# Kernel tuning notes

Measured on AMD Instinct MI355X. Metric: run time of the kernel, lower is better.

## Reference

```python
import jax, jax.numpy as jnp
import numpy as np

FP8_MAX = 448.0  # max normal for float8_e4m3fn
BLOCK = 128


def setup_inputs() -> dict:
    key = jax.random.key(0)
    k1, k2, k3 = jax.random.split(key, 3)
    B, S, D_IN, D_OUT = 2, 2048, 4096, 8192
    x = jax.random.normal(k1, (B, S, D_IN), dtype=jnp.float32)
    # stored weight is fp8_e4m3fn; materialize as f32 values that are exactly fp8-representable
    w = jax.random.normal(k2, (D_OUT, D_IN), dtype=jnp.float32)
    weight = w.astype(jnp.float8_e4m3fn).astype(jnp.float32)
    # positive per-(128x128)-block dequant scales
    weight_scale_inv = (
        jax.random.uniform(k3, (D_OUT // BLOCK, D_IN // BLOCK), dtype=jnp.float32) * 0.05 + 0.005
    )
    return {"x": x, "weight": weight, "weight_scale_inv": weight_scale_inv}


def _quantize_per_token(x2d):
    # x2d: [M, K] -> fp8 values + [M, 1] f32 scale
    amax = jnp.clip(jnp.max(jnp.abs(x2d), axis=-1, keepdims=True), min=1e-12)
    x_scale = (amax / FP8_MAX).astype(jnp.float32)
    x_fp8 = (x2d / x_scale).astype(jnp.float8_e4m3fn)
    return x_fp8, x_scale


def _dequantize_weight(weight, weight_scale_inv):
    # weight: [O, K] (fp8-representable f32), scales: [O/B, K/B]
    O, K = weight.shape
    w_fp8 = weight.astype(jnp.float8_e4m3fn).astype(jnp.float32)
    wb = w_fp8.reshape(O // BLOCK, BLOCK, K // BLOCK, BLOCK)
    wb = wb * weight_scale_inv[:, None, :, None]
    return wb.reshape(O, K)


def reference(x, weight, weight_scale_inv):
    orig_shape = x.shape
    x2d = x.reshape(-1, orig_shape[-1])  # [M, K], M > 1 path
    x_fp8, x_scale = _quantize_per_token(x2d)
    # block-scaled fp8 GEMM: y[m,n] = x_scale[m] * sum_k x_fp8[m,k] * w_fp8[n,k] * s[n//B,k//B]
    w_deq = _dequantize_weight(weight, weight_scale_inv)  # [O, K]
    y = jnp.einsum("mk,ok->mo", x_fp8.astype(jnp.float32), w_deq) * x_scale
    return y.reshape(*orig_shape[:-1], weight.shape[0])
```

## Files before the change

### kernel.cpp

```cpp
#include <hip/hip_runtime.h>

typedef float f32x4  __attribute__((ext_vector_type(4)));
typedef float f32x16 __attribute__((ext_vector_type(16)));
typedef int   i32x4  __attribute__((ext_vector_type(4)));
typedef int   i32x8  __attribute__((ext_vector_type(8)));

#define AS1 __attribute__((address_space(1)))
#define AS3 __attribute__((address_space(3)))

__global__ __launch_bounds__(256) void quant_x_fp8_kernel(
    const float* __restrict__ x, unsigned char* __restrict__ x8,
    float* __restrict__ xs, int K) {
  int m = blockIdx.x;
  int t = threadIdx.x;
  const f32x4* src = (const f32x4*)(x + (size_t)m * K + t * 16);
  f32x4 v[4];
  float am = 0.0f;
#pragma unroll
  for (int i = 0; i < 4; ++i) {
    v[i] = src[i];
#pragma unroll
    for (int j = 0; j < 4; ++j) am = fmaxf(am, __builtin_fabsf(v[i][j]));
  }
#pragma unroll
  for (int off = 32; off >= 1; off >>= 1)
    am = fmaxf(am, __shfl_xor(am, off, 64));
  __shared__ float red[4];
  int wv = t >> 6, lane = t & 63;
  if (lane == 0) red[wv] = am;
  __syncthreads();
  am = fmaxf(fmaxf(red[0], red[1]), fmaxf(red[2], red[3]));
  am = fmaxf(am, 1e-12f);
  float sc = am / 448.0f;
  if (t == 0) xs[m] = sc;
  i32x4 out;
#pragma unroll
  for (int i = 0; i < 4; ++i) {
    float q0 = v[i][0] / sc, q1 = v[i][1] / sc;
    float q2 = v[i][2] / sc, q3 = v[i][3] / sc;
    int p = __builtin_amdgcn_cvt_pk_fp8_f32(q0, q1, 0, false);
    p = __builtin_amdgcn_cvt_pk_fp8_f32(q2, q3, p, true);
    out[i] = p;
  }
  *(i32x4*)(x8 + (size_t)m * K + t * 16) = out;
}

__global__ __launch_bounds__(256) void quant_w_fp8_kernel(
    const float* __restrict__ w, unsigned char* __restrict__ w8) {
  size_t idx = (size_t)blockIdx.x * 256 + threadIdx.x;
  const f32x4* src = (const f32x4*)w + idx * 4;
  i32x4 out;
#pragma unroll
  for (int i = 0; i < 4; ++i) {
    f32x4 v = src[i];
    int p = __builtin_amdgcn_cvt_pk_fp8_f32(v[0], v[1], 0, false);
    p = __builtin_amdgcn_cvt_pk_fp8_f32(v[2], v[3], p, true);
    out[i] = p;
  }
  ((i32x4*)w8)[idx] = out;
}

__global__ __launch_bounds__(256, 2) void gemm_mxfp8_kernel(
    const unsigned char* __restrict__ A8,
    const unsigned char* __restrict__ W8,
    const float* __restrict__ xs,
    const float* __restrict__ wsinv,
    float* __restrict__ Y,
    int M, int N, int K) {
  const int KB = K >> 7;

  int bid = blockIdx.x, nwg = gridDim.x;
  int wg = (bid & 7) * (nwg >> 3) + (bid >> 3);
  int mt = M >> 8;
  int bm = wg & (mt - 1);
  int bn = wg / mt;
  int m0 = bm << 8, n0 = bn << 7;

  __shared__ __align__(16) char lds[49152];

  const int tid = threadIdx.x, wv = tid >> 6, lane = tid & 63;
  const int wr = wv >> 1, wc = wv & 1;
  const int l31 = lane & 31, hi2 = lane >> 5;

  const int lineB = (l31 >> 1) * 128;
  const int par4 = (l31 & 1) << 2;
  const int xr = (l31 >> 1) & 7;
  const int s0 = 2 * hi2, s1 = 2 * hi2 + 1;
  const int aL = wr * 8192 + lineB + ((par4 | s0) ^ xr) * 16;
  const int aH = wr * 8192 + lineB + ((par4 | s1) ^ xr) * 16;
  const int bL = wc * 4096 + lineB + ((par4 | s0) ^ xr) * 16;
  const int bH = wc * 4096 + lineB + ((par4 | s1) ^ xr) * 16;

  const int stgD = tid << 4;
  const int inv = (tid & 7) ^ ((tid >> 3) & 7);
  const int rLoc = 2 * (tid >> 3) + (inv >> 2);
  const int cSrc = (inv & 3) << 4;
  const size_t rowB = (size_t)K;
  const size_t g64r = 64 * rowB;
  const char* pA = (const char*)A8 + (size_t)(m0 + rLoc) * rowB + cSrc;
  const char* pB = (const char*)W8 + (size_t)(n0 + rLoc) * rowB + cSrc;

  const float* wsv = wsinv + (size_t)bn * KB;

  f32x16 acc[4][2];
#pragma unroll
  for (int i = 0; i < 4; ++i)
#pragma unroll
    for (int j = 0; j < 2; ++j) acc[i][j] = (f32x16)0.0f;

  i32x8 af, bf[2];

#define GL(SRC, DST)                                                           \
  __builtin_amdgcn_global_load_lds((const AS1 void*)(SRC), (AS3 void*)(DST),   \
                                   16, 0, 0)
#define STG_A(COND, SB, SRC)                                                   \
  if (COND) {                                                                  \
    const char* s_ = (SRC);                                                    \
    char* d_ = lds + (SB) + stgD;                                              \
    GL(s_, d_);                                                                \
    GL(s_ + g64r, d_ + 4096);                                                  \
    GL(s_ + 2 * g64r, d_ + 8192);                                              \
    GL(s_ + 3 * g64r, d_ + 12288);                                             \
  }
#define STG_B(COND, SB, SRC)                                                   \
  if (COND) {                                                                  \
    const char* s_ = (SRC);                                                    \
    char* d_ = lds + (SB) + 16384 + stgD;                                      \
    GL(s_, d_);                                                                \
    GL(s_ + g64r, d_ + 4096);                                                  \
  }

#define RD_A(RB, MJ)                                                           \
  {                                                                            \
    const char* p_ = lds + (RB) + (MJ) * 2048;                                 \
    i32x4 lo = *(const i32x4*)(p_ + aL);                                       \
    i32x4 hi = *(const i32x4*)(p_ + aH);                                       \
    af = __builtin_shufflevector(lo, hi, 0, 1, 2, 3, 4, 5, 6, 7);              \
  }
#define RD_B(RB, NJ)                                                           \
  {                                                                            \
    const char* p_ = lds + (RB) + 16384 + (NJ) * 2048;                         \
    i32x4 lo = *(const i32x4*)(p_ + bL);                                       \
    i32x4 hi = *(const i32x4*)(p_ + bH);                                       \
    bf[NJ] = __builtin_shufflevector(lo, hi, 0, 1, 2, 3, 4, 5, 6, 7);          \
  }

#define MMFF(MJ, NJ, R_)                                                       \
  {                                                                            \
    _Pragma("unroll") for (int q = 0; q < 16; ++q)                             \
        acc[MJ][NJ][q] *= (R_);                                                \
    acc[MJ][NJ] = __builtin_amdgcn_mfma_scale_f32_32x32x64_f8f6f4(             \
        af, bf[NJ], acc[MJ][NJ], 0, 0, 0, 0x7f7f7f7f, 0, 0x7f7f7f7f);          \
  }
#define MMFD(MJ, NJ)                                                           \
  acc[MJ][NJ] = __builtin_amdgcn_mfma_scale_f32_32x32x64_f8f6f4(               \
      af, bf[NJ], acc[MJ][NJ], 0, 0, 0, 0x7f7f7f7f, 0, 0x7f7f7f7f);

#define BODY_CORE(MM0, MM1, MM2, MM3, RD, ST, G)                               \
  {                                                                            \
    RD_B(RD, 0);                                                               \
    RD_B(RD, 1);                                                               \
    RD_A(RD, 0);                                                               \
    STG_A(G, ST, pAs);                                                         \
    __builtin_amdgcn_s_setprio(1);                                             \
    MM0;                                                                       \
    __builtin_amdgcn_s_setprio(0);                                             \
    STG_B(G, ST, pBs);                                                         \
    RD_A(RD, 1);                                                               \
    __builtin_amdgcn_s_setprio(1);                                             \
    MM1;                                                                       \
    __builtin_amdgcn_s_setprio(0);                                             \
    RD_A(RD, 2);                                                               \
    __builtin_amdgcn_s_setprio(1);                                             \
    MM2;                                                                       \
    __builtin_amdgcn_s_setprio(0);                                             \
    RD_A(RD, 3);                                                               \
    __builtin_amdgcn_s_setprio(1);                                             \
    MM3;                                                                       \
    __builtin_amdgcn_s_setprio(0);                                             \
    asm volatile("s_waitcnt vmcnt(0)" ::: "memory");                           \
    __builtin_amdgcn_s_barrier();                                              \
    pAs += 64;                                                                 \
    pBs += 64;                                                                 \
  }

#define BODY_E(T, G)                                                           \
  {                                                                            \
    float sc_ = wsv[(T)];                                                      \
    float r_ = sp_ / sc_;                                                      \
    sp_ = sc_;                                                                 \
    BODY_CORE(MMFF(0, 0, r_); MMFF(0, 1, r_), MMFF(1, 0, r_); MMFF(1, 1, r_),  \
              MMFF(2, 0, r_); MMFF(2, 1, r_), MMFF(3, 0, r_); MMFF(3, 1, r_),  \
              0, 24576, G)                                                     \
  }
#define BODY_O(G)                                                              \
  BODY_CORE(MMFD(0, 0); MMFD(0, 1), MMFD(1, 0); MMFD(1, 1),                    \
            MMFD(2, 0); MMFD(2, 1), MMFD(3, 0); MMFD(3, 1), 24576, 0, G)

  STG_A(true, 0, pA);
  STG_B(true, 0, pB);
  asm volatile("s_waitcnt vmcnt(0)" ::: "memory");
  __builtin_amdgcn_s_barrier();

  const char* pAs = pA + 64;
  const char* pBs = pB + 64;
  float sp_ = wsv[0];

#pragma unroll 1
  for (int t = 0; t < KB; ++t) {
    BODY_E(t, true)
    BODY_O(t < KB - 1)
  }

#undef BODY_O
#undef BODY_E
#undef BODY_CORE
#undef MMFD
#undef MMFF
#undef RD_B
#undef RD_A
#undef STG_B
#undef STG_A
#undef GL

  const float sl_ = sp_;
#pragma unroll
  for (int mj = 0; mj < 4; ++mj)
#pragma unroll
    for (int nj = 0; nj < 2; ++nj) {
      int col = n0 + wc * 64 + nj * 32 + l31;
#pragma unroll
      for (int q = 0; q < 4; ++q) {
        int row0 = m0 + wr * 128 + mj * 32 + q * 8 + hi2 * 4;
        f32x4 sv = *(const f32x4*)(xs + row0);
#pragma unroll
        for (int j = 0; j < 4; ++j)
          Y[(size_t)(row0 + j) * N + col] = acc[mj][nj][q * 4 + j] * sv[j] * sl_;
      }
    }
}

extern "C" void kernel_launch(void* const* d_in, const int* in_sizes, int n_in,
                              void* d_out, int out_size, void* d_ws, size_t ws_size,
                              hipStream_t stream) {
  const float* x     = (const float*)d_in[0];
  const float* w     = (const float*)d_in[1];
  const float* wsinv = (const float*)d_in[2];
  float* y = (float*)d_out;

  const int K = 4096;
  const int M = in_sizes[0] / K;
  const int N = in_sizes[1] / K;

  unsigned char* x8 = (unsigned char*)d_ws;
  float* xs = (float*)((char*)d_ws + (size_t)M * K);
  unsigned char* w8 =
      (unsigned char*)d_ws + (size_t)M * K + (size_t)M * 4;

  quant_x_fp8_kernel<<<M, 256, 0, stream>>>(x, x8, xs, K);
  quant_w_fp8_kernel<<<(int)(((size_t)N * K / 16 + 255) / 256), 256, 0,
                       stream>>>(w, w8);

  dim3 grid((M / 256) * (N / 128));
  gemm_mxfp8_kernel<<<grid, 256, 0, stream>>>(x8, w8, xs, wsinv, y, M, N, K);
}
```

Measured before the change: 217.7 us.

## Triple-buffer A tiles in LDS and deepen prefetch with partial vmcnt waits

Grows LDS to 64KB and moves from a double-buffered combined A/B stage to a three-slot ring for A plus a separate two-slot region for B. A tiles are now prefetched two half-steps ahead, and the barrier waits only until at most 4 loads are outstanding instead of draining all of them, so global loads overlap more with MFMA work. The loop is unrolled by three to rotate the buffers, with a hardcoded trip count of 30 plus a tail, which assumes K=4096. The larger LDS footprint may reduce occupancy below the two blocks per CU declared in launch bounds.

```diff
diff --git a/kernel.cpp b/kernel.cpp
--- a/kernel.cpp
+++ b/kernel.cpp
@@ -76,7 +76,7 @@
   int bn = wg / mt;
   int m0 = bm << 8, n0 = bn << 7;
 
-  __shared__ __align__(16) char lds[49152];
+  __shared__ __align__(16) char lds[65536];
 
   const int tid = threadIdx.x, wv = tid >> 6, lane = tid & 63;
   const int wr = wv >> 1, wc = wv & 1;
@@ -125,7 +125,7 @@
 #define STG_B(COND, SB, SRC)                                                   \
   if (COND) {                                                                  \
     const char* s_ = (SRC);                                                    \
-    char* d_ = lds + (SB) + 16384 + stgD;                                      \
+    char* d_ = lds + (SB) + stgD;                                              \
     GL(s_, d_);                                                                \
     GL(s_ + g64r, d_ + 4096);                                                  \
   }
@@ -139,7 +139,7 @@
   }
 #define RD_B(RB, NJ)                                                           \
   {                                                                            \
-    const char* p_ = lds + (RB) + 16384 + (NJ) * 2048;                         \
+    const char* p_ = lds + (RB) + (NJ) * 2048;                                 \
     i32x4 lo = *(const i32x4*)(p_ + bL);                                       \
     i32x4 hi = *(const i32x4*)(p_ + bH);                                       \
     bf[NJ] = __builtin_shufflevector(lo, hi, 0, 1, 2, 3, 4, 5, 6, 7);          \
@@ -156,61 +156,72 @@
   acc[MJ][NJ] = __builtin_amdgcn_mfma_scale_f32_32x32x64_f8f6f4(               \
       af, bf[NJ], acc[MJ][NJ], 0, 0, 0, 0x7f7f7f7f, 0, 0x7f7f7f7f);
 
-#define BODY_CORE(MM0, MM1, MM2, MM3, RD, ST, G)                               \
-  {                                                                            \
-    RD_B(RD, 0);                                                               \
-    RD_B(RD, 1);                                                               \
-    RD_A(RD, 0);                                                               \
-    STG_A(G, ST, pAs);                                                         \
+#define BODY_CORE(MM0, MM1, MM2, MM3, AR, BR, BS, AS, GB, GA, VM)              \
+  {                                                                            \
+    RD_B(BR, 0);                                                               \
+    RD_B(BR, 1);                                                               \
+    RD_A(AR, 0);                                                               \
+    STG_B(GB, BS, pBs);                                                        \
+    STG_A(GA, AS, pAs);                                                        \
     __builtin_amdgcn_s_setprio(1);                                             \
     MM0;                                                                       \
     __builtin_amdgcn_s_setprio(0);                                             \
-    STG_B(G, ST, pBs);                                                         \
-    RD_A(RD, 1);                                                               \
+    RD_A(AR, 1);                                                               \
     __builtin_amdgcn_s_setprio(1);                                             \
     MM1;                                                                       \
     __builtin_amdgcn_s_setprio(0);                                             \
-    RD_A(RD, 2);                                                               \
+    RD_A(AR, 2);                                                               \
     __builtin_amdgcn_s_setprio(1);                                             \
     MM2;                                                                       \
     __builtin_amdgcn_s_setprio(0);                                             \
-    RD_A(RD, 3);                                                               \
+    RD_A(AR, 3);                                                               \
     __builtin_amdgcn_s_setprio(1);                                             \
     MM3;                                                                       \
     __builtin_amdgcn_s_setprio(0);                                             \
-    asm volatile("s_waitcnt vmcnt(0)" ::: "memory");                           \
+    asm volatile("s_waitcnt " VM ::: "memory");                                \
     __builtin_amdgcn_s_barrier();                                              \
     pAs += 64;                                                                 \
     pBs += 64;                                                                 \
   }
 
-#define BODY_E(T, G)                                                           \
-  {                                                                            \
-    float sc_ = wsv[(T)];                                                      \
+#define BODY_E(SC_, AR, BR, BS, AS, GB, GA, VM)                                \
+  {                                                                            \
+    float sc_ = (SC_);                                                         \
     float r_ = sp_ / sc_;                                                      \
     sp_ = sc_;                                                                 \
     BODY_CORE(MMFF(0, 0, r_); MMFF(0, 1, r_), MMFF(1, 0, r_); MMFF(1, 1, r_),  \
               MMFF(2, 0, r_); MMFF(2, 1, r_), MMFF(3, 0, r_); MMFF(3, 1, r_),  \
-              0, 24576, G)                                                     \
-  }
-#define BODY_O(G)                                                              \
+              AR, BR, BS, AS, GB, GA, VM)                                      \
+  }
+#define BODY_O(AR, BR, BS, AS, GB, GA, VM)                                     \
   BODY_CORE(MMFD(0, 0); MMFD(0, 1), MMFD(1, 0); MMFD(1, 1),                    \
-            MMFD(2, 0); MMFD(2, 1), MMFD(3, 0); MMFD(3, 1), 24576, 0, G)
+            MMFD(2, 0); MMFD(2, 1), MMFD(3, 0); MMFD(3, 1),                    \
+            AR, BR, BS, AS, GB, GA, VM)
 
   STG_A(true, 0, pA);
-  STG_B(true, 0, pB);
-  asm volatile("s_waitcnt vmcnt(0)" ::: "memory");
+  STG_B(true, 49152, pB);
+  STG_A(true, 16384, pA + 64);
+  asm volatile("s_waitcnt vmcnt(4)" ::: "memory");
   __builtin_amdgcn_s_barrier();
 
-  const char* pAs = pA + 64;
+  const char* pAs = pA + 128;
   const char* pBs = pB + 64;
   float sp_ = wsv[0];
 
 #pragma unroll 1
-  for (int t = 0; t < KB; ++t) {
-    BODY_E(t, true)
-    BODY_O(t < KB - 1)
-  }
+  for (int t0 = 0; t0 < 30; t0 += 3) {
+    float sA_ = wsv[t0], sB_ = wsv[t0 + 1], sC_ = wsv[t0 + 2];
+    BODY_E(sA_, 0,     49152, 57344, 32768, true, true, "vmcnt(4)")
+    BODY_O(     16384, 57344, 49152, 0,     true, true, "vmcnt(4)")
+    BODY_E(sB_, 32768, 49152, 57344, 16384, true, true, "vmcnt(4)")
+    BODY_O(     0,     57344, 49152, 32768, true, true, "vmcnt(4)")
+    BODY_E(sC_, 16384, 49152, 57344, 0,     true, true, "vmcnt(4)")
+    BODY_O(     32768, 57344, 49152, 16384, true, true, "vmcnt(4)")
+  }
+  BODY_E(wsv[30], 0,     49152, 57344, 32768, true,  true,  "vmcnt(4)")
+  BODY_O(         16384, 57344, 49152, 0,     true,  true,  "vmcnt(4)")
+  BODY_E(wsv[31], 32768, 49152, 57344, 0,     true,  false, "vmcnt(0)")
+  BODY_O(         0,     57344, 49152, 0,     false, false, "vmcnt(0)")
 
 #undef BODY_O
 #undef BODY_E
```

After: 211.5 us. -2.9%, faster.
